# Kernel tuning notes

Hardware: AMD Instinct MI355X
Metric: run time of the kernel (lower is better)

Reference implementation:

```python
import jax, jax.numpy as jnp
import numpy as np

NUM_EXPERTS = 8
TOP_K = 2
ROUTE_SCALE = 1.0
DIM = 1024
HID = 1024
B, S = 2, 4096


def setup_inputs() -> dict:
    key = jax.random.key(0)
    ks = jax.random.split(key, 9)
    sc = 0.05
    return {
        "x": jax.random.normal(ks[0], (B, S, DIM), dtype=jnp.float32),
        "gate_w": jax.random.normal(ks[1], (NUM_EXPERTS, DIM), dtype=jnp.float32) * sc,
        "w1": jax.random.normal(ks[2], (NUM_EXPERTS, HID, DIM), dtype=jnp.float32) * sc,
        "w2": jax.random.normal(ks[3], (NUM_EXPERTS, DIM, HID), dtype=jnp.float32) * sc,
        "w3": jax.random.normal(ks[4], (NUM_EXPERTS, HID, DIM), dtype=jnp.float32) * sc,
        "sw1": jax.random.normal(ks[5], (HID, DIM), dtype=jnp.float32) * sc,
        "sw2": jax.random.normal(ks[6], (DIM, HID), dtype=jnp.float32) * sc,
        "sw3": jax.random.normal(ks[7], (HID, DIM), dtype=jnp.float32) * sc,
        "expert_bias": jnp.zeros((NUM_EXPERTS,), dtype=jnp.float32),
    }


def reference(x, gate_w, w1, w2, w3, sw1, sw2, sw3, expert_bias):
    bs, slen, dim = x.shape
    xf = x.reshape(-1, dim)                      # [T, D]

    # ---- router (sigmoid scoring, top-k over scores + bias, gather true scores) ----
    scores = jax.nn.sigmoid((xf @ gate_w.T).astype(jnp.float32))   # [T, E]
    _, sel = jax.lax.top_k(scores + expert_bias[None, :], TOP_K)    # [T, K] int32
    top_scores = jnp.take_along_axis(scores, sel, axis=1) * ROUTE_SCALE  # [T, K]

    # ---- stable sort token-slots by chosen expert (dispatch permutation) ----
    flat_sel = sel.reshape(-1)                       # [T*K]
    order = jnp.argsort(flat_sel, stable=True)       # [T*K]
    scores_sorted = top_scores.reshape(-1)[order]    # [T*K]
    tok_idx = order // TOP_K                         # source token per slot
    expert_ids = flat_sel[order]                     # sorted expert id per slot

    routed = xf[tok_idx]                             # gather [T*K, D]
    # score_before_experts=True: scale inputs by routing score
    routed = (routed.astype(jnp.float32) * scores_sorted[:, None]).astype(x.dtype)

    # ---- grouped expert GLU MLP (loop over fixed expert count, masked) ----
    out_r = jnp.zeros_like(routed)
    for e in range(NUM_EXPERTS):
        m = (expert_ids == e)[:, None]
        h = jax.nn.silu(routed @ w1[e].T) * (routed @ w3[e].T)   # [T*K, H]
        out_r = out_r + jnp.where(m, h @ w2[e].T, jnp.zeros((), routed.dtype))

    # ---- shared expert on all tokens ----
    shared = (jax.nn.silu(xf @ sw1.T) * (xf @ sw3.T)) @ sw2.T    # [T, D]

    # NOTE: original code multiplies by routing scores again after experts
    # (in addition to score_before_experts) -- replicated faithfully.
    out_r = (out_r.astype(jnp.float32) * scores_sorted[:, None]).astype(x.dtype)

    out = shared.at[tok_idx].add(out_r)              # scatter-add combine
    return out.reshape(bs, slen, dim)
```

## Files before the change

### kernel.cpp

```cpp
#include <hip/hip_runtime.h>
#include <stdint.h>

typedef unsigned short u16;
typedef unsigned int u32;

#define T_TOK 8192
#define DIMSZ 1024
#define HIDSZ 1024
#define NE 8
#define NSLOT (T_TOK * 2)
#define NPAD (NSLOT + 1024)

typedef __attribute__((ext_vector_type(8))) __bf16 bf16x8;
typedef __attribute__((ext_vector_type(4))) float f32x4;

__device__ __forceinline__ size_t ablk(int pos, int c) {
  return ((((size_t)(pos >> 7) * 32 + (c >> 5)) * 4 + ((c >> 3) & 3)) * 128 +
          (pos & 127)) * 8 + (c & 7);
}

__device__ __forceinline__ u16 f2bf(float f) {
  u32 u = __builtin_bit_cast(u32, f);
  u += 0x7FFFu + ((u >> 16) & 1u);
  return (u16)(u >> 16);
}
__device__ __forceinline__ float bflo(u32 v) { return __builtin_bit_cast(float, v << 16); }
__device__ __forceinline__ float bfhi(u32 v) { return __builtin_bit_cast(float, v & 0xffff0000u); }
__device__ __forceinline__ u32 pack2(float a, float b) {
  return (u32)f2bf(a) | ((u32)f2bf(b) << 16);
}
__device__ __forceinline__ float silu_f(float v) { return v / (1.f + expf(-v)); }

__global__ __launch_bounds__(256) void convert_blocked(
    const float* __restrict__ s0, const float* __restrict__ s1,
    const float* __restrict__ s2, u16* __restrict__ d0, u16* __restrict__ d1,
    u16* __restrict__ d2) {
  const float* s = (blockIdx.y == 0) ? s0 : (blockIdx.y == 1) ? s1 : s2;
  u16* d = (blockIdx.y == 0) ? d0 : (blockIdx.y == 1) ? d1 : d2;
  __shared__ u16 lt[2048];
  int t = blockIdx.x;
  int rt = t >> 5, kt = t & 31;
  const float* sp = s + (size_t)rt * 64 * 1024 + kt * 32;
  int nl = threadIdx.x >> 2, k0 = (threadIdx.x & 3) * 8;
  float4 a = *(const float4*)(sp + (size_t)nl * 1024 + k0);
  float4 b = *(const float4*)(sp + (size_t)nl * 1024 + k0 + 4);
  uint4 p;
  p.x = pack2(a.x, a.y); p.y = pack2(a.z, a.w);
  p.z = pack2(b.x, b.y); p.w = pack2(b.z, b.w);
  *(uint4*)&lt[(threadIdx.x & 3) * 512 + nl * 8] = p;
  __syncthreads();
  *(uint4*)(d + (size_t)t * 2048 + threadIdx.x * 8) = *(const uint4*)&lt[threadIdx.x * 8];
}

__global__ __launch_bounds__(256) void router_kernel(
    const float* __restrict__ x, const float* __restrict__ gw,
    const float* __restrict__ bias, int* __restrict__ sel,
    float* __restrict__ selscore, u16* __restrict__ xb) {
  int t = blockIdx.x * 4 + (threadIdx.x >> 6);
  int lane = threadIdx.x & 63;
  float a[NE];
#pragma unroll
  for (int e = 0; e < NE; e++) a[e] = 0.f;
#pragma unroll
  for (int j = 0; j < 4; j++) {
    int c = j * 256 + lane * 4;
    float4 xv = *(const float4*)&x[(size_t)t * DIMSZ + c];
    uint2 p;
    p.x = pack2(xv.x, xv.y);
    p.y = pack2(xv.z, xv.w);
    *(uint2*)&xb[ablk(t, c)] = p;
#pragma unroll
    for (int e = 0; e < NE; e++) {
      float4 gv = *(const float4*)&gw[e * DIMSZ + c];
      a[e] = fmaf(xv.x, gv.x, fmaf(xv.y, gv.y, fmaf(xv.z, gv.z, fmaf(xv.w, gv.w, a[e]))));
    }
  }
#pragma unroll
  for (int off = 1; off < 64; off <<= 1)
#pragma unroll
    for (int e = 0; e < NE; e++) a[e] += __shfl_xor(a[e], off);
  if (lane == 0) {
    float s[NE], b[NE];
#pragma unroll
    for (int e = 0; e < NE; e++) {
      s[e] = 1.f / (1.f + expf(-a[e]));
      b[e] = s[e] + bias[e];
    }
    int e1 = 0; float v1 = b[0];
#pragma unroll
    for (int e = 1; e < NE; e++) if (b[e] > v1) { v1 = b[e]; e1 = e; }
    int e2 = -1; float v2 = -1e30f;
#pragma unroll
    for (int e = 0; e < NE; e++) if (e != e1 && b[e] > v2) { v2 = b[e]; e2 = e; }
    sel[t * 2] = e1; sel[t * 2 + 1] = e2;
    selscore[t * 2] = s[e1];
    selscore[t * 2 + 1] = s[e2];
  }
}

__global__ __launch_bounds__(1024) void rank_kernel(
    const int* __restrict__ sel, const float* __restrict__ selscore,
    int* __restrict__ slot2pos, float* __restrict__ slot_score,
    int* __restrict__ counts, int* __restrict__ offsets) {
  __shared__ int hist[NE * 1024];
  __shared__ int tot[NE];
  __shared__ int offs[NE];
  int tid = threadIdx.x;
  int sl[16];
  int h[NE];
#pragma unroll
  for (int e = 0; e < NE; e++) h[e] = 0;
#pragma unroll
  for (int j = 0; j < 4; j++) {
    int4 v = ((const int4*)sel)[tid * 4 + j];
    sl[j * 4 + 0] = v.x; sl[j * 4 + 1] = v.y;
    sl[j * 4 + 2] = v.z; sl[j * 4 + 3] = v.w;
  }
#pragma unroll
  for (int i = 0; i < 16; i++)
#pragma unroll
    for (int e = 0; e < NE; e++) h[e] += (sl[i] == e) ? 1 : 0;
#pragma unroll
  for (int e = 0; e < NE; e++) hist[e * 1024 + tid] = h[e];
  __syncthreads();
  int wid = tid >> 6, lane = tid & 63;
  if (wid < NE) {
    int e = wid;
    int vals[16];
    int lsum = 0;
#pragma unroll
    for (int i = 0; i < 16; i++) {
      int v = hist[e * 1024 + lane * 16 + i];
      vals[i] = lsum;
      lsum += v;
    }
    int incl = lsum;
#pragma unroll
    for (int off = 1; off < 64; off <<= 1) {
      int v = __shfl_up(incl, off);
      if (lane >= off) incl += v;
    }
    int excl = incl - lsum;
#pragma unroll
    for (int i = 0; i < 16; i++) hist[e * 1024 + lane * 16 + i] = vals[i] + excl;
    if (lane == 63) tot[e] = incl;
  }
  __syncthreads();
  if (tid == 0) {
    int acc = 0;
    for (int e = 0; e < NE; e++) {
      offs[e] = acc;
      offsets[e] = acc;
      counts[e] = tot[e];
      acc += (tot[e] + 127) & ~127;
    }
  }
  __syncthreads();
  int base[NE];
#pragma unroll
  for (int e = 0; e < NE; e++) base[e] = offs[e] + hist[e * 1024 + tid];
#pragma unroll
  for (int i = 0; i < 16; i++) {
    int slot = tid * 16 + i;
    int e = sl[i];
    int pos = 0;
#pragma unroll
    for (int k = 0; k < NE; k++) pos += (e == k) ? base[k] : 0;
#pragma unroll
    for (int k = 0; k < NE; k++) base[k] += (e == k) ? 1 : 0;
    slot2pos[slot] = pos;
    slot_score[pos] = selscore[slot];
  }
}

__global__ __launch_bounds__(256) void gather_kernel(
    const float* __restrict__ x, const float* __restrict__ selscore,
    const int* __restrict__ slot2pos, u16* __restrict__ routed) {
  int s = blockIdx.x * 4 + (threadIdx.x >> 6);
  int lane = threadIdx.x & 63;
  int pos = slot2pos[s];
  float sc = selscore[s];
  int t = s >> 1;
#pragma unroll
  for (int j = 0; j < 4; j++) {
    int c = j * 256 + lane * 4;
    float4 v = *(const float4*)&x[(size_t)t * DIMSZ + c];
    uint2 p;
    p.x = pack2(v.x * sc, v.y * sc);
    p.y = pack2(v.z * sc, v.w * sc);
    *(uint2*)&routed[ablk(pos, c)] = p;
  }
}

__global__ __launch_bounds__(256) void dual_glu_gemm(
    const u16* __restrict__ A, const u16* __restrict__ W1,
    const u16* __restrict__ W3, u16* __restrict__ Hout,
    const u16* __restrict__ As, const u16* __restrict__ SW1,
    const u16* __restrict__ SW3, u16* __restrict__ Hs,
    const int* __restrict__ seg_off, const int* __restrict__ seg_cnt) {
  int z = blockIdx.z;
  const u16 *Ap, *w1p, *w3p;
  u16* Hp;
  int soff, scnt;
  if (z < NE) {
    soff = seg_off[z]; scnt = seg_cnt[z];
    Ap = A;
    w1p = W1 + (size_t)z * HIDSZ * DIMSZ;
    w3p = W3 + (size_t)z * HIDSZ * DIMSZ;
    Hp = Hout;
  } else {
    soff = 0; scnt = T_TOK;
    Ap = As; w1p = SW1; w3p = SW3;
    Hp = Hs;
  }
  int mbase = blockIdx.y * 128;
  if (mbase >= scnt) return;
  int nbase = blockIdx.x * 64;

  __shared__ u16 lA[4096];
  __shared__ u16 lB1[2048];
  __shared__ u16 lB3[2048];

  int tid = threadIdx.x;
  int lane = tid & 63;
  int wid = tid >> 6;
  int wy = wid >> 1, wx = wid & 1;
  int q = lane >> 4, lm = lane & 15;

  f32x4 acc1[4][2], acc3[4][2];
#pragma unroll
  for (int i = 0; i < 4; i++)
#pragma unroll
    for (int j = 0; j < 2; j++) { acc1[i][j] = (f32x4)0.f; acc3[i][j] = (f32x4)0.f; }

  const u16* gA = Ap + ((size_t)((soff + mbase) >> 7) * 32) * 4096 + tid * 8;
  const u16* gB1 = w1p + ((size_t)(nbase >> 6) * 32) * 2048 + tid * 8;
  const u16* gB3 = w3p + ((size_t)(nbase >> 6) * 32) * 2048 + tid * 8;

  for (int kt = 0; kt < DIMSZ / 32; kt++) {
    uint4 vA0 = *(const uint4*)gA;
    uint4 vA1 = *(const uint4*)(gA + 2048);
    uint4 v1 = *(const uint4*)gB1;
    uint4 v3 = *(const uint4*)gB3;
    gA += 4096; gB1 += 2048; gB3 += 2048;
    *(uint4*)&lA[tid * 8] = vA0;
    *(uint4*)&lA[2048 + tid * 8] = vA1;
    *(uint4*)&lB1[tid * 8] = v1;
    *(uint4*)&lB3[tid * 8] = v3;
    __syncthreads();
    bf16x8 af[4];
#pragma unroll
    for (int i = 0; i < 4; i++)
      af[i] = *(const bf16x8*)&lA[(q * 128 + wy * 64 + i * 16 + lm) * 8];
    bf16x8 b1f[2], b3f[2];
#pragma unroll
    for (int j = 0; j < 2; j++) {
      int col = wx * 32 + j * 16 + lm;
      b1f[j] = *(const bf16x8*)&lB1[(q * 64 + col) * 8];
      b3f[j] = *(const bf16x8*)&lB3[(q * 64 + col) * 8];
    }
#pragma unroll
    for (int i = 0; i < 4; i++)
#pragma unroll
      for (int j = 0; j < 2; j++) {
        acc1[i][j] = __builtin_amdgcn_mfma_f32_16x16x32_bf16(af[i], b1f[j], acc1[i][j], 0, 0, 0);
        acc3[i][j] = __builtin_amdgcn_mfma_f32_16x16x32_bf16(af[i], b3f[j], acc3[i][j], 0, 0, 0);
      }
    __syncthreads();
  }
#pragma unroll
  for (int i = 0; i < 4; i++) {
    int rowb = mbase + wy * 64 + i * 16 + q * 4;
#pragma unroll
    for (int j = 0; j < 2; j++) {
      int col = nbase + wx * 32 + j * 16 + lm;
      f32x4 g1 = acc1[i][j], g3 = acc3[i][j];
#pragma unroll
      for (int rr = 0; rr < 4; rr++) {
        int grow = rowb + rr;
        if (grow < scnt)
          Hp[ablk(soff + grow, col)] = f2bf(silu_f(g1[rr]) * g3[rr]);
      }
    }
  }
}

__global__ __launch_bounds__(256) void gemm2_kernel(
    const u16* __restrict__ A, const u16* __restrict__ W, u16* __restrict__ OutB,
    const u16* __restrict__ As, const u16* __restrict__ SW, float* __restrict__ OutF,
    const float* __restrict__ scale, const int* __restrict__ seg_off,
    const int* __restrict__ seg_cnt) {
  int z = blockIdx.z;
  const u16 *Ap, *wp;
  int soff, scnt;
  if (z < NE) {
    soff = seg_off[z]; scnt = seg_cnt[z];
    Ap = A; wp = W + (size_t)z * DIMSZ * HIDSZ;
  } else {
    soff = 0; scnt = T_TOK;
    Ap = As; wp = SW;
  }
  int mbase = blockIdx.y * 128;
  if (mbase >= scnt) return;
  int nbase = blockIdx.x * 128;

  __shared__ u16 lA[4096];
  __shared__ u16 lB[4096];

  int tid = threadIdx.x;
  int lane = tid & 63;
  int wid = tid >> 6;
  int wy = wid >> 1, wx = wid & 1;
  int q = lane >> 4, lm = lane & 15;

  f32x4 acc[4][4];
#pragma unroll
  for (int i = 0; i < 4; i++)
#pragma unroll
    for (int j = 0; j < 4; j++) acc[i][j] = (f32x4)0.f;

  const u16* gA = Ap + ((size_t)((soff + mbase) >> 7) * 32) * 4096 + tid * 8;
  const u16* gB0 = wp + ((size_t)(nbase >> 6) * 32) * 2048 + tid * 8;
  const u16* gB1 = wp + ((size_t)((nbase >> 6) + 1) * 32) * 2048 + tid * 8;

  for (int kt = 0; kt < HIDSZ / 32; kt++) {
    uint4 vA0 = *(const uint4*)gA;
    uint4 vA1 = *(const uint4*)(gA + 2048);
    uint4 vB0 = *(const uint4*)gB0;
    uint4 vB1 = *(const uint4*)gB1;
    gA += 4096; gB0 += 2048; gB1 += 2048;
    *(uint4*)&lA[tid * 8] = vA0;
    *(uint4*)&lA[2048 + tid * 8] = vA1;
    *(uint4*)&lB[tid * 8] = vB0;
    *(uint4*)&lB[2048 + tid * 8] = vB1;
    __syncthreads();
    bf16x8 af[4], bf[4];
#pragma unroll
    for (int i = 0; i < 4; i++) {
      af[i] = *(const bf16x8*)&lA[(q * 128 + wy * 64 + i * 16 + lm) * 8];
      bf[i] = *(const bf16x8*)&lB[wx * 2048 + (q * 64 + i * 16 + lm) * 8];
    }
#pragma unroll
    for (int i = 0; i < 4; i++)
#pragma unroll
      for (int j = 0; j < 4; j++)
        acc[i][j] = __builtin_amdgcn_mfma_f32_16x16x32_bf16(af[i], bf[j], acc[i][j], 0, 0, 0);
    __syncthreads();
  }
#pragma unroll
  for (int i = 0; i < 4; i++) {
    int rowb = mbase + wy * 64 + i * 16 + q * 4;
#pragma unroll
    for (int j = 0; j < 4; j++) {
      int col = nbase + wx * 64 + j * 16 + lm;
      f32x4 a = acc[i][j];
#pragma unroll
      for (int rr = 0; rr < 4; rr++) {
        int grow = rowb + rr;
        if (grow < scnt) {
          size_t idx = (size_t)(soff + grow) * DIMSZ + col;
          if (z < NE) {
            OutB[idx] = f2bf(a[rr] * scale[soff + grow]);
          } else {
            OutF[idx] = a[rr];
          }
        }
      }
    }
  }
}

__global__ __launch_bounds__(256) void combine_kernel(
    float* __restrict__ out, const u16* __restrict__ Orb,
    const int* __restrict__ slot2pos) {
  int t = blockIdx.x;
  int d = threadIdx.x * 4;
  int p0 = slot2pos[t * 2];
  int p1 = slot2pos[t * 2 + 1];
  float4 o = *(float4*)&out[(size_t)t * DIMSZ + d];
  uint2 a = *(const uint2*)&Orb[(size_t)p0 * DIMSZ + d];
  uint2 b = *(const uint2*)&Orb[(size_t)p1 * DIMSZ + d];
  o.x += bflo(a.x) + bflo(b.x);
  o.y += bfhi(a.x) + bfhi(b.x);
  o.z += bflo(a.y) + bflo(b.y);
  o.w += bfhi(a.y) + bfhi(b.y);
  *(float4*)&out[(size_t)t * DIMSZ + d] = o;
}

extern "C" void kernel_launch(void* const* d_in, const int* in_sizes, int n_in,
                              void* d_out, int out_size, void* d_ws, size_t ws_size,
                              hipStream_t stream) {
  const float* x = (const float*)d_in[0];
  const float* gw = (const float*)d_in[1];
  const float* w1 = (const float*)d_in[2];
  const float* w2 = (const float*)d_in[3];
  const float* w3 = (const float*)d_in[4];
  const float* sw1 = (const float*)d_in[5];
  const float* sw2 = (const float*)d_in[6];
  const float* sw3 = (const float*)d_in[7];
  const float* bias = (const float*)d_in[8];
  float* out = (float*)d_out;

  uint8_t* ws = (uint8_t*)d_ws;
  size_t off = 0;
  auto alloc = [&](size_t b) { size_t o = off; off += (b + 255) & ~(size_t)255; return o; };

  size_t ctrl = alloc(256);
  int* counts = (int*)(ws + ctrl);
  int* offsets = counts + 16;
  int* sel = (int*)(ws + alloc((size_t)NSLOT * 4));
  float* selscore = (float*)(ws + alloc((size_t)NSLOT * 4));
  float* slot_score = (float*)(ws + alloc((size_t)NPAD * 4));
  int* slot2pos = (int*)(ws + alloc((size_t)NSLOT * 4));
  u16* xb = (u16*)(ws + alloc((size_t)T_TOK * DIMSZ * 2));
  u16* routed = (u16*)(ws + alloc((size_t)NPAD * DIMSZ * 2));
  u16* Hbuf = (u16*)(ws + alloc((size_t)NPAD * HIDSZ * 2));
  u16* Orb = (u16*)(ws + alloc((size_t)NPAD * DIMSZ * 2));
  u16* Hs = (u16*)(ws + alloc((size_t)T_TOK * HIDSZ * 2));
  u16* w1b = (u16*)(ws + alloc((size_t)NE * HIDSZ * DIMSZ * 2));
  u16* w2b = (u16*)(ws + alloc((size_t)NE * DIMSZ * HIDSZ * 2));
  u16* w3b = (u16*)(ws + alloc((size_t)NE * HIDSZ * DIMSZ * 2));
  u16* sw1b = (u16*)(ws + alloc((size_t)HIDSZ * DIMSZ * 2));
  u16* sw2b = (u16*)(ws + alloc((size_t)DIMSZ * HIDSZ * 2));
  u16* sw3b = (u16*)(ws + alloc((size_t)HIDSZ * DIMSZ * 2));

  convert_blocked<<<dim3(NE * 16 * 32, 3), 256, 0, stream>>>(
      w1, w2, w3, w1b, w2b, w3b);
  convert_blocked<<<dim3(16 * 32, 3), 256, 0, stream>>>(
      sw1, sw2, sw3, sw1b, sw2b, sw3b);

  router_kernel<<<T_TOK / 4, 256, 0, stream>>>(x, gw, bias, sel, selscore, xb);
  rank_kernel<<<1, 1024, 0, stream>>>(sel, selscore, slot2pos, slot_score,
                                      counts, offsets);
  gather_kernel<<<NSLOT / 4, 256, 0, stream>>>(x, selscore, slot2pos, routed);

  dual_glu_gemm<<<dim3(16, 64, NE + 1), 256, 0, stream>>>(
      routed, w1b, w3b, Hbuf, xb, sw1b, sw3b, Hs, offsets, counts);
  gemm2_kernel<<<dim3(8, 64, NE + 1), 256, 0, stream>>>(
      Hbuf, w2b, Orb, Hs, sw2b, out, slot_score, offsets, counts);

  combine_kernel<<<T_TOK, 256, 0, stream>>>(out, Orb, slot2pos);
}
```

Before: 541.7 us.

## Double-buffer LDS tiles and prefetch next K-tile in both expert GEMMs

Both grouped GEMM kernels now use two LDS buffers and issue global loads for the next K-tile into registers right after the barrier. Those loads are in flight while the MFMAs run on the current tile, and the trailing barrier goes away because each iteration writes the other buffer. This hides global load latency and cuts one barrier per iteration, at the cost of twice the LDS and more live registers, which may lower occupancy.

```diff
diff --git a/kernel.cpp b/kernel.cpp
--- a/kernel.cpp
+++ b/kernel.cpp
@@ -217,9 +217,9 @@
   if (mbase >= scnt) return;
   int nbase = blockIdx.x * 64;
 
-  __shared__ u16 lA[4096];
-  __shared__ u16 lB1[2048];
-  __shared__ u16 lB3[2048];
+  __shared__ u16 lA[2][4096];
+  __shared__ u16 lB1[2][2048];
+  __shared__ u16 lB3[2][2048];
 
   int tid = threadIdx.x;
   int lane = tid & 63;
@@ -237,27 +237,36 @@
   const u16* gB1 = w1p + ((size_t)(nbase >> 6) * 32) * 2048 + tid * 8;
   const u16* gB3 = w3p + ((size_t)(nbase >> 6) * 32) * 2048 + tid * 8;
 
+  uint4 rA0 = *(const uint4*)gA;
+  uint4 rA1 = *(const uint4*)(gA + 2048);
+  uint4 rB1 = *(const uint4*)gB1;
+  uint4 rB3 = *(const uint4*)gB3;
+  gA += 4096; gB1 += 2048; gB3 += 2048;
+
   for (int kt = 0; kt < DIMSZ / 32; kt++) {
-    uint4 vA0 = *(const uint4*)gA;
-    uint4 vA1 = *(const uint4*)(gA + 2048);
-    uint4 v1 = *(const uint4*)gB1;
-    uint4 v3 = *(const uint4*)gB3;
-    gA += 4096; gB1 += 2048; gB3 += 2048;
-    *(uint4*)&lA[tid * 8] = vA0;
-    *(uint4*)&lA[2048 + tid * 8] = vA1;
-    *(uint4*)&lB1[tid * 8] = v1;
-    *(uint4*)&lB3[tid * 8] = v3;
+    int buf = kt & 1;
+    *(uint4*)&lA[buf][tid * 8] = rA0;
+    *(uint4*)&lA[buf][2048 + tid * 8] = rA1;
+    *(uint4*)&lB1[buf][tid * 8] = rB1;
+    *(uint4*)&lB3[buf][tid * 8] = rB3;
     __syncthreads();
+    if (kt < DIMSZ / 32 - 1) {
+      rA0 = *(const uint4*)gA;
+      rA1 = *(const uint4*)(gA + 2048);
+      rB1 = *(const uint4*)gB1;
+      rB3 = *(const uint4*)gB3;
+      gA += 4096; gB1 += 2048; gB3 += 2048;
+    }
     bf16x8 af[4];
 #pragma unroll
     for (int i = 0; i < 4; i++)
-      af[i] = *(const bf16x8*)&lA[(q * 128 + wy * 64 + i * 16 + lm) * 8];
+      af[i] = *(const bf16x8*)&lA[buf][(q * 128 + wy * 64 + i * 16 + lm) * 8];
     bf16x8 b1f[2], b3f[2];
 #pragma unroll
     for (int j = 0; j < 2; j++) {
       int col = wx * 32 + j * 16 + lm;
-      b1f[j] = *(const bf16x8*)&lB1[(q * 64 + col) * 8];
-      b3f[j] = *(const bf16x8*)&lB3[(q * 64 + col) * 8];
+      b1f[j] = *(const bf16x8*)&lB1[buf][(q * 64 + col) * 8];
+      b3f[j] = *(const bf16x8*)&lB3[buf][(q * 64 + col) * 8];
     }
 #pragma unroll
     for (int i = 0; i < 4; i++)
@@ -266,7 +275,6 @@
         acc1[i][j] = __builtin_amdgcn_mfma_f32_16x16x32_bf16(af[i], b1f[j], acc1[i][j], 0, 0, 0);
         acc3[i][j] = __builtin_amdgcn_mfma_f32_16x16x32_bf16(af[i], b3f[j], acc3[i][j], 0, 0, 0);
       }
-    __syncthreads();
   }
 #pragma unroll
   for (int i = 0; i < 4; i++) {
@@ -304,8 +312,8 @@
   if (mbase >= scnt) return;
   int nbase = blockIdx.x * 128;
 
-  __shared__ u16 lA[4096];
-  __shared__ u16 lB[4096];
+  __shared__ u16 lA[2][4096];
+  __shared__ u16 lB[2][4096];
 
   int tid = threadIdx.x;
   int lane = tid & 63;
@@ -323,29 +331,37 @@
   const u16* gB0 = wp + ((size_t)(nbase >> 6) * 32) * 2048 + tid * 8;
   const u16* gB1 = wp + ((size_t)((nbase >> 6) + 1) * 32) * 2048 + tid * 8;
 
+  uint4 rA0 = *(const uint4*)gA;
+  uint4 rA1 = *(const uint4*)(gA + 2048);
+  uint4 rB0 = *(const uint4*)gB0;
+  uint4 rB1 = *(const uint4*)gB1;
+  gA += 4096; gB0 += 2048; gB1 += 2048;
+
   for (int kt = 0; kt < HIDSZ / 32; kt++) {
-    uint4 vA0 = *(const uint4*)gA;
-    uint4 vA1 = *(const uint4*)(gA + 2048);
-    uint4 vB0 = *(const uint4*)gB0;
-    uint4 vB1 = *(const uint4*)gB1;
-    gA += 4096; gB0 += 2048; gB1 += 2048;
-    *(uint4*)&lA[tid * 8] = vA0;
-    *(uint4*)&lA[2048 + tid * 8] = vA1;
-    *(uint4*)&lB[tid * 8] = vB0;
-    *(uint4*)&lB[2048 + tid * 8] = vB1;
+    int buf = kt & 1;
+    *(uint4*)&lA[buf][tid * 8] = rA0;
+    *(uint4*)&lA[buf][2048 + tid * 8] = rA1;
+    *(uint4*)&lB[buf][tid * 8] = rB0;
+    *(uint4*)&lB[buf][2048 + tid * 8] = rB1;
     __syncthreads();
+    if (kt < HIDSZ / 32 - 1) {
+      rA0 = *(const uint4*)gA;
+      rA1 = *(const uint4*)(gA + 2048);
+      rB0 = *(const uint4*)gB0;
+      rB1 = *(const uint4*)gB1;
+      gA += 4096; gB0 += 2048; gB1 += 2048;
+    }
     bf16x8 af[4], bf[4];
 #pragma unroll
     for (int i = 0; i < 4; i++) {
-      af[i] = *(const bf16x8*)&lA[(q * 128 + wy * 64 + i * 16 + lm) * 8];
-      bf[i] = *(const bf16x8*)&lB[wx * 2048 + (q * 64 + i * 16 + lm) * 8];
+      af[i] = *(const bf16x8*)&lA[buf][(q * 128 + wy * 64 + i * 16 + lm) * 8];
+      bf[i] = *(const bf16x8*)&lB[buf][wx * 2048 + (q * 64 + i * 16 + lm) * 8];
     }
 #pragma unroll
     for (int i = 0; i < 4; i++)
 #pragma unroll
       for (int j = 0; j < 4; j++)
         acc[i][j] = __builtin_amdgcn_mfma_f32_16x16x32_bf16(af[i], bf[j], acc[i][j], 0, 0, 0);
-    __syncthreads();
   }
 #pragma unroll
   for (int i = 0; i < 4; i++) {
```

Measured after the change: 524.7 us. -3.1%, faster.
